# Kernel optimization log

Measured on AMD Instinct MI355X. Metric: run time of the kernel, lower is better.

## Reference

```python
import jax, jax.numpy as jnp
import numpy as np

THRESHOLD = 20.0
CIRCLE_OFFSETS = [(0, -3), (1, -3), (2, -2), (3, -1), (3, 0), (3, 1), (2, 2), (1, 3),
                  (0, 3), (-1, 3), (-2, 2), (-3, 1), (-3, 0), (-3, -1), (-2, -2), (-1, -3)]


def setup_inputs() -> dict:
    key = jax.random.key(0)
    image = jax.random.uniform(key, (4, 1, 1080, 1920), dtype=jnp.float32) * 255.0
    return {"image": image}


def _detect_9_consecutive(bits_16):
    # bits_16: int32 (N, H, W). Build 24-bit circular buffer, test all 16 rotations
    # for 9 consecutive set bits (window == 511) using arithmetic-only ops.
    lower_8 = bits_16 % 256
    buffer_24 = bits_16 + lower_8 * 65536  # (N, H, W) int32
    divisors = (jnp.int32(2) ** jnp.arange(16, dtype=jnp.int32)).reshape(16, 1, 1, 1)
    shifted = (buffer_24[None] // divisors) % 512  # (16, N, H, W)
    return jnp.any(shifted == 511, axis=0)  # (N, H, W) bool


def reference(image):
    N, C, H, W = image.shape
    img = image.astype(jnp.float32)
    # Replicate-pad by 3 and gather the 16 Bresenham circle pixels via shifted slices.
    padded = jnp.pad(img[:, 0], ((0, 0), (3, 3), (3, 3)), mode='edge')  # (N, H+6, W+6)
    circle = jnp.stack(
        [padded[:, 3 + dy:3 + dy + H, 3 + dx:3 + dx + W] for dy, dx in CIRCLE_OFFSETS],
        axis=-1)  # (N, H, W, 16)
    center = img[:, 0][..., None]  # (N, H, W, 1)
    diff = circle - center
    powers = (jnp.int32(1) << jnp.arange(16, dtype=jnp.int32)).reshape(1, 1, 1, 16)
    dark_bits = ((diff >= THRESHOLD).astype(jnp.int32) * powers).sum(axis=-1)
    bright_bits = ((diff <= -THRESHOLD).astype(jnp.int32) * powers).sum(axis=-1)
    detected = _detect_9_consecutive(dark_bits) | _detect_9_consecutive(bright_bits)
    return detected.astype(jnp.float32)[:, None]  # (N, 1, H, W)
```

## Files before the change

### kernel.cpp

```cpp
#include <hip/hip_runtime.h>

#define IMG_H 1080
#define IMG_W 1920

__device__ __forceinline__ unsigned det9(unsigned m) {
    unsigned x = m | (m << 16);
    unsigned t = x & (x >> 1);
    t &= t >> 2;
    t &= t >> 4;
    t &= x >> 8;
    return t;
}

#define STEP_GE(m, sc, val, thr)                                          \
    asm("v_cmp_ge_f32 %1, %2, %3\n\tv_addc_co_u32 %0, %1, %0, %0, %1"     \
        : "+v"(m), "=s"(sc) : "v"(val), "v"(thr))
#define STEP_LE(m, sc, val, thr)                                          \
    asm("v_cmp_le_f32 %1, %2, %3\n\tv_addc_co_u32 %0, %1, %0, %0, %1"     \
        : "+v"(m), "=s"(sc) : "v"(val), "v"(thr))

__global__ __launch_bounds__(256) void fast_score_kernel(const float* __restrict__ img,
                                                         float* __restrict__ out) {
    const int n  = blockIdx.z;
    const int y  = blockIdx.y;
    const int gx = blockIdx.x * 256 + threadIdx.x;

    const float* base = img + (size_t)n * (IMG_H * IMG_W);

    const float* rp[7];
#pragma unroll
    for (int d = 0; d < 7; ++d) {
        const int ry = min(max(y + d - 3, 0), IMG_H - 1);
        rp[d] = base + (size_t)ry * IMG_W;
    }

    int c[7];
#pragma unroll
    for (int d = 0; d < 7; ++d) {
        c[d] = min(max(gx + d - 3, 0), IMG_W - 1);
    }

    constexpr int DY[16] = {0, 1, 2, 3, 3, 3, 2, 1, 0, -1, -2, -3, -3, -3, -2, -1};
    constexpr int DX[16] = {-3, -3, -2, -1, 0, 1, 2, 3, 3, 3, 2, 1, 0, -1, -2, -3};

    const float center = rp[3][c[3]];
    float t[16];
#pragma unroll
    for (int k = 0; k < 16; ++k) {
        t[k] = rp[DY[k] + 3][c[DX[k] + 3]];
    }

    const float hi = center + 20.0f;
    const float lo = center - 20.0f;
    unsigned dark = 0u, bright = 0u;
    unsigned long long sc0, sc1;
#pragma unroll
    for (int k = 0; k < 16; ++k) {
        STEP_GE(dark,   sc0, t[k], hi);
        STEP_LE(bright, sc1, t[k], lo);
    }

    const float res = (det9(dark) | det9(bright)) ? 1.0f : 0.0f;
    if (gx < IMG_W) {
        out[(size_t)n * (IMG_H * IMG_W) + (size_t)y * IMG_W + gx] = res;
    }
}

extern "C" void kernel_launch(void* const* d_in, const int* in_sizes, int n_in,
                              void* d_out, int out_size, void* d_ws, size_t ws_size,
                              hipStream_t stream) {
    const float* img = (const float*)d_in[0];
    float* out = (float*)d_out;
    const int n_img = in_sizes[0] / (IMG_H * IMG_W);
    dim3 grid((IMG_W + 255) / 256,
              IMG_H,
              n_img);
    fast_score_kernel<<<grid, 256, 0, stream>>>(img, out);
}
```

Measured before the change: 99.27 us.

## Compute four pixels per thread with vectorized inline-asm row loads

Each thread now handles four adjacent output pixels, gathering the 7-row stencil with 128-bit (and 64-bit) global loads in inline asm so neighbouring columns share loaded values, and writes a float4 result. Border threads fall back to the clamped scalar path. This cuts the number of load instructions and address computations per pixel, at the cost of more registers per thread and a grid reduced to two blocks per row.

```diff
diff --git a/kernel.cpp b/kernel.cpp
--- a/kernel.cpp
+++ b/kernel.cpp
@@ -2,6 +2,9 @@
 
 #define IMG_H 1080
 #define IMG_W 1920
+
+typedef float f32x4 __attribute__((ext_vector_type(4)));
+typedef float f32x2 __attribute__((ext_vector_type(2)));
 
 __device__ __forceinline__ unsigned det9(unsigned m) {
     unsigned x = m | (m << 16);
@@ -19,50 +22,124 @@
     asm("v_cmp_le_f32 %1, %2, %3\n\tv_addc_co_u32 %0, %1, %0, %0, %1"     \
         : "+v"(m), "=s"(sc) : "v"(val), "v"(thr))
 
+constexpr int DY[16] = {0, 1, 2, 3, 3, 3, 2, 1, 0, -1, -2, -3, -3, -3, -2, -1};
+constexpr int DX[16] = {-3, -3, -2, -1, 0, 1, 2, 3, 3, 3, 2, 1, 0, -1, -2, -3};
+
 __global__ __launch_bounds__(256) void fast_score_kernel(const float* __restrict__ img,
                                                          float* __restrict__ out) {
     const int n  = blockIdx.z;
     const int y  = blockIdx.y;
-    const int gx = blockIdx.x * 256 + threadIdx.x;
+    const int x0 = (blockIdx.x * 256 + threadIdx.x) * 4;
+    if (x0 >= IMG_W) return;
 
     const float* base = img + (size_t)n * (IMG_H * IMG_W);
+    float* ob = out + (size_t)n * (IMG_H * IMG_W) + (size_t)y * IMG_W;
 
-    const float* rp[7];
+    const float* rp0 = base + (size_t)min(max(y - 3, 0), IMG_H - 1) * IMG_W;
+    const float* rp1 = base + (size_t)min(max(y - 2, 0), IMG_H - 1) * IMG_W;
+    const float* rp2 = base + (size_t)min(max(y - 1, 0), IMG_H - 1) * IMG_W;
+    const float* rp3 = base + (size_t)y * IMG_W;
+    const float* rp4 = base + (size_t)min(y + 1, IMG_H - 1) * IMG_W;
+    const float* rp5 = base + (size_t)min(y + 2, IMG_H - 1) * IMG_W;
+    const float* rp6 = base + (size_t)min(y + 3, IMG_H - 1) * IMG_W;
+
+    if (x0 >= 4 && x0 <= IMG_W - 8) {
+        const unsigned xm3 = (unsigned)(x0 - 3) * 4u;
+        const unsigned xm2 = (unsigned)(x0 - 2) * 4u;
+        const unsigned xm1 = (unsigned)(x0 - 1) * 4u;
+        const unsigned xc  = (unsigned)(x0)     * 4u;
+        const unsigned xp2 = (unsigned)(x0 + 2) * 4u;
+        const unsigned xp3 = (unsigned)(x0 + 3) * 4u;
+
+        f32x4 ra3, ra2, ra2b, ra1, ra1b, r0a, r0c, r0b, rc1, rc1b, rc2, rc2b, rc3;
+        f32x2 ra3b, rc3b;
+        asm volatile(
+            "global_load_dwordx4 %0,  %17, %21\n\t"
+            "global_load_dwordx2 %1,  %20, %21\n\t"
+            "global_load_dwordx4 %2,  %16, %22\n\t"
+            "global_load_dwordx4 %3,  %19, %22\n\t"
+            "global_load_dwordx4 %4,  %15, %23\n\t"
+            "global_load_dwordx4 %5,  %20, %23\n\t"
+            "global_load_dwordx4 %6,  %15, %24\n\t"
+            "global_load_dwordx4 %7,  %18, %24\n\t"
+            "global_load_dwordx4 %8,  %20, %24\n\t"
+            "global_load_dwordx4 %9,  %15, %25\n\t"
+            "global_load_dwordx4 %10, %20, %25\n\t"
+            "global_load_dwordx4 %11, %16, %26\n\t"
+            "global_load_dwordx4 %12, %19, %26\n\t"
+            "global_load_dwordx4 %13, %17, %27\n\t"
+            "global_load_dwordx2 %14, %20, %27\n\t"
+            "s_waitcnt vmcnt(0)"
+            : "=&v"(ra3), "=&v"(ra3b), "=&v"(ra2), "=&v"(ra2b), "=&v"(ra1),
+              "=&v"(ra1b), "=&v"(r0a), "=&v"(r0c), "=&v"(r0b), "=&v"(rc1),
+              "=&v"(rc1b), "=&v"(rc2), "=&v"(rc2b), "=&v"(rc3), "=&v"(rc3b)
+            : "v"(xm3), "v"(xm2), "v"(xm1), "v"(xc), "v"(xp2), "v"(xp3),
+              "s"(rp0), "s"(rp1), "s"(rp2), "s"(rp3), "s"(rp4), "s"(rp5), "s"(rp6));
+
+        float res[4];
 #pragma unroll
-    for (int d = 0; d < 7; ++d) {
-        const int ry = min(max(y + d - 3, 0), IMG_H - 1);
-        rp[d] = base + (size_t)ry * IMG_W;
-    }
+        for (int p = 0; p < 4; ++p) {
+            const float top1 = (p + 0) < 4 ? ra3[p + 0] : ra3b[p - 4];
+            const float top2 = (p + 1) < 4 ? ra3[p + 1] : ra3b[p - 3];
+            const float top3 = (p + 2) < 4 ? ra3[p + 2] : ra3b[p - 2];
+            const float bot1 = (p + 0) < 4 ? rc3[p + 0] : rc3b[p - 4];
+            const float bot2 = (p + 1) < 4 ? rc3[p + 1] : rc3b[p - 3];
+            const float bot3 = (p + 2) < 4 ? rc3[p + 2] : rc3b[p - 2];
 
-    int c[7];
+            const float t[16] = {
+                r0a[p],
+                rc1[p],
+                rc2[p],
+                bot1,
+                bot2,
+                bot3,
+                rc2b[p],
+                rc1b[p],
+                r0b[p],
+                ra1b[p],
+                ra2b[p],
+                top3,
+                top2,
+                top1,
+                ra2[p],
+                ra1[p],
+            };
+            const float center = r0c[p];
+            const float hi = center + 20.0f;
+            const float lo = center - 20.0f;
+            unsigned dark = 0u, bright = 0u;
+            unsigned long long sc0, sc1;
 #pragma unroll
-    for (int d = 0; d < 7; ++d) {
-        c[d] = min(max(gx + d - 3, 0), IMG_W - 1);
-    }
-
-    constexpr int DY[16] = {0, 1, 2, 3, 3, 3, 2, 1, 0, -1, -2, -3, -3, -3, -2, -1};
-    constexpr int DX[16] = {-3, -3, -2, -1, 0, 1, 2, 3, 3, 3, 2, 1, 0, -1, -2, -3};
-
-    const float center = rp[3][c[3]];
-    float t[16];
+            for (int k = 0; k < 16; ++k) {
+                STEP_GE(dark,   sc0, t[k], hi);
+                STEP_LE(bright, sc1, t[k], lo);
+            }
+            res[p] = (det9(dark) | det9(bright)) ? 1.0f : 0.0f;
+        }
+        *(float4*)(ob + x0) = make_float4(res[0], res[1], res[2], res[3]);
+    } else {
+        const float* rp[7] = {rp0, rp1, rp2, rp3, rp4, rp5, rp6};
 #pragma unroll
-    for (int k = 0; k < 16; ++k) {
-        t[k] = rp[DY[k] + 3][c[DX[k] + 3]];
-    }
-
-    const float hi = center + 20.0f;
-    const float lo = center - 20.0f;
-    unsigned dark = 0u, bright = 0u;
-    unsigned long long sc0, sc1;
+        for (int p = 0; p < 4; ++p) {
+            const int col = x0 + p;
+            const float center = rp[3][col];
+            float t[16];
 #pragma unroll
-    for (int k = 0; k < 16; ++k) {
-        STEP_GE(dark,   sc0, t[k], hi);
-        STEP_LE(bright, sc1, t[k], lo);
-    }
-
-    const float res = (det9(dark) | det9(bright)) ? 1.0f : 0.0f;
-    if (gx < IMG_W) {
-        out[(size_t)n * (IMG_H * IMG_W) + (size_t)y * IMG_W + gx] = res;
+            for (int k = 0; k < 16; ++k) {
+                const int cc = min(max(col + DX[k], 0), IMG_W - 1);
+                t[k] = rp[DY[k] + 3][cc];
+            }
+            const float hi = center + 20.0f;
+            const float lo = center - 20.0f;
+            unsigned dark = 0u, bright = 0u;
+            unsigned long long sc0, sc1;
+#pragma unroll
+            for (int k = 0; k < 16; ++k) {
+                STEP_GE(dark,   sc0, t[k], hi);
+                STEP_LE(bright, sc1, t[k], lo);
+            }
+            ob[col] = (det9(dark) | det9(bright)) ? 1.0f : 0.0f;
+        }
     }
 }
 
@@ -72,7 +149,7 @@
     const float* img = (const float*)d_in[0];
     float* out = (float*)d_out;
     const int n_img = in_sizes[0] / (IMG_H * IMG_W);
-    dim3 grid((IMG_W + 255) / 256,
+    dim3 grid(2,
               IMG_H,
               n_img);
     fast_score_kernel<<<grid, 256, 0, stream>>>(img, out);
```

After: 104.5 us. +5.3%, slower.
